# Kernel optimization log

Measured on AMD Instinct MI355X. Metric: run time of the kernel, lower is better.

Reference implementation:

```python
import jax, jax.numpy as jnp
import numpy as np


def setup_inputs() -> dict:
    key = jax.random.key(0)
    k1, k2 = jax.random.split(key)
    N, B, E, H = 2048, 8, 256, 512
    x = jax.random.normal(k1, (N, B, E), dtype=jnp.float32)
    h = jax.random.normal(k2, (N, B, H), dtype=jnp.float32)
    return {"x": x, "h": h}


def reference(x, h):
    # x: (N, B, E), h: (N, B, H)
    H = h.shape[-1]
    xt = jnp.transpose(x, (1, 0, 2))            # (B, N, E)
    norm = jnp.linalg.norm(xt, axis=2, keepdims=True)  # (B, N, 1)
    xn = xt / norm
    # cosine-similarity scores, softmax over keys (last dim)
    scores = jax.nn.softmax(jnp.einsum('bie,bje->bij', xn, xn), axis=2)  # (B, N, N)
    ht = jnp.transpose(h, (1, 0, 2))            # (B, N, H)
    # The original expands scores/h over an H-fold dim, bmm's, and sums;
    # that equals H * (scores @ h). Keep the H factor for faithfulness
    # (it cancels in the global-norm division below).
    g = H * jnp.einsum('bij,bjh->bih', scores, ht)  # (B, N, H)
    g = jnp.transpose(g, (1, 0, 2))             # (N, B, H)
    return g / jnp.linalg.norm(g)
```

## Files before the change

kernel.cpp:

```cpp
#include <hip/hip_runtime.h>

#define N_TOK 2048
#define B_SZ  8
#define E_DIM 256
#define H_DIM 512
#define ITERS (N_TOK / 32)
#define QROWS 64

typedef __attribute__((ext_vector_type(8))) short bf16x8;
typedef __attribute__((ext_vector_type(4))) float f32x4;
typedef __attribute__((ext_vector_type(4))) unsigned short u16x4;

__device__ __forceinline__ unsigned short f2bf(float f) {
    union { float f; unsigned u; } v; v.f = f;
    unsigned r = v.u + 0x7FFF + ((v.u >> 16) & 1);
    return (unsigned short)(r >> 16);
}
__device__ __forceinline__ float bf2f(unsigned short b) {
    union { unsigned u; float f; } v; v.u = ((unsigned)b) << 16;
    return v.f;
}

__global__ void prep_kernel(const float* __restrict__ x,
                            const float* __restrict__ hptr,
                            unsigned short* __restrict__ Xn,
                            unsigned short* __restrict__ Vp,
                            float* __restrict__ sumsq) {
    int bid = blockIdx.x;
    int t = threadIdx.x;
    if (bid == 0 && t == 0) *sumsq = 0.0f;
    if (bid < (N_TOK * B_SZ) / 4) {
        int w = t >> 6, lane = t & 63;
        int r = bid * 4 + w;
        int n = r >> 3, b = r & 7;
        float4 v = *(const float4*)(x + (size_t)r * E_DIM + lane * 4);
        float s = v.x * v.x + v.y * v.y + v.z * v.z + v.w * v.w;
        #pragma unroll
        for (int o = 32; o > 0; o >>= 1) s += __shfl_xor(s, o);
        float rn = 1.0f / sqrtf(s);
        u16x4 pk;
        pk[0] = f2bf(v.x * rn); pk[1] = f2bf(v.y * rn);
        pk[2] = f2bf(v.z * rn); pk[3] = f2bf(v.w * rn);
        int u = lane >> 1, half = lane & 1;
        *(u16x4*)(Xn + ((size_t)b * N_TOK + n) * E_DIM
                     + (size_t)((u ^ (n & 7)) * 8 + half * 4)) = pk;
    } else {
        int lin = bid - (N_TOK * B_SZ) / 4;
        int jb = lin & 63, hb = (lin >> 6) & 15, b = lin >> 10;
        __shared__ __attribute__((aligned(16))) float tile[32][36];
        int j0 = jb * 32, h0 = hb * 32;
        {
            int j = t >> 3, c = (t & 7) * 4;
            float4 v = *(const float4*)(hptr +
                ((size_t)(j0 + j) * B_SZ + b) * H_DIM + h0 + c);
            *(float4*)(&tile[j][c]) = v;
        }
        __syncthreads();
        size_t base = ((size_t)b * (N_TOK / 32) + jb) * (H_DIM * 32);
        int hcl = t >> 3, jg = (t >> 1) & 3, half = t & 1;
        int hc = h0 + hcl;
        u16x4 pk;
        #pragma unroll
        for (int k = 0; k < 4; k++)
            pk[k] = f2bf(tile[jg * 8 + half * 4 + k][hcl]);
        *(u16x4*)(Vp + base + (size_t)(hc * 4 + (jg ^ ((hcl >> 1) & 3))) * 8
                     + half * 4) = pk;
    }
}

#define PT_STRIDE 40

__launch_bounds__(256, 2)
__global__ void flash_kernel(const unsigned short* __restrict__ Xn,
                             const unsigned short* __restrict__ Vp,
                             float* __restrict__ out,
                             float* __restrict__ sumsq) {
    __shared__ __attribute__((aligned(16))) unsigned short Kbuf[2][32 * 256];
    __shared__ __attribute__((aligned(16))) unsigned short Pt[4][16 * PT_STRIDE];
    __shared__ float Lred[4][16];

    int b  = blockIdx.x;
    int q0 = blockIdx.y * QROWS;
    int z  = blockIdx.z;
    int t = threadIdx.x;
    int w = t >> 6, lane = t & 63;
    int quad = lane >> 4, nm = lane & 15;

    const unsigned short* Kbase = Xn + (size_t)b * N_TOK * E_DIM;
    const unsigned short* Qrow =
        Xn + ((size_t)b * N_TOK + q0 + w * 16 + nm) * E_DIM;
    const unsigned short* Vtile0 = Vp + (size_t)b * (N_TOK / 32) * (H_DIM * 32);
    int col0 = z * 256 + w * 64;

    bf16x8 qf[8];
    #pragma unroll
    for (int ec = 0; ec < 8; ec++)
        qf[ec] = *(const bf16x8*)(Qrow + (size_t)(((ec * 4 + quad) ^ (nm & 7)) * 8));

    f32x4 O[4][4];
    #pragma unroll
    for (int i = 0; i < 4; i++)
        #pragma unroll
        for (int j = 0; j < 4; j++) O[i][j] = (f32x4){0.f, 0.f, 0.f, 0.f};
    float l_lane[4];
    #pragma unroll
    for (int r = 0; r < 4; r++) l_lane[r] = 0.0f;

    auto stage = [&](int tile, int buf) {
        const unsigned short* src0 = Kbase + (size_t)tile * 32 * E_DIM;
        #pragma unroll
        for (int k = 0; k < 4; k++) {
            int chunk = w * 4 + k;
            __builtin_amdgcn_global_load_lds(
                (const __attribute__((address_space(1))) unsigned int*)
                    (src0 + (size_t)chunk * 512 + lane * 8),
                (__attribute__((address_space(3))) unsigned int*)
                    (&Kbuf[buf][chunk * 512]),
                16, 0, 0);
        }
    };

    stage(0, 0);
    int vswz = (quad ^ ((nm >> 1) & 3)) * 8;

    for (int it = 0; it < ITERS; ++it) {
        __syncthreads();
        int cur = it & 1;

        const unsigned short* Vt = Vtile0 + (size_t)it * (H_DIM * 32);
        bf16x8 vf[4];
        #pragma unroll
        for (int tt = 0; tt < 4; tt++) {
            int hc = col0 + tt * 16 + nm;
            vf[tt] = *(const bf16x8*)(Vt + (size_t)(hc * 4) * 8 + vswz);
        }

        if (it + 1 < ITERS) stage(it + 1, cur ^ 1);
        const unsigned short* KB = &Kbuf[cur][0];

        f32x4 sa = (f32x4){0.f,0.f,0.f,0.f}, sb = (f32x4){0.f,0.f,0.f,0.f};
        #pragma unroll
        for (int ec = 0; ec < 8; ec++) {
            int u = ((ec * 4 + quad) ^ (nm & 7)) * 8;
            bf16x8 kf0 = *(const bf16x8*)(KB + nm * 256 + u);
            bf16x8 kf1 = *(const bf16x8*)(KB + (16 + nm) * 256 + u);
            sa = __builtin_amdgcn_mfma_f32_16x16x32_bf16(qf[ec], kf0, sa, 0, 0, 0);
            sb = __builtin_amdgcn_mfma_f32_16x16x32_bf16(qf[ec], kf1, sb, 0, 0, 0);
        }

        #pragma unroll
        for (int r = 0; r < 4; r++) {
            unsigned short pb0 = f2bf(__expf(sa[r] - 1.0f));
            unsigned short pb1 = f2bf(__expf(sb[r] - 1.0f));
            l_lane[r] += bf2f(pb0) + bf2f(pb1);
            Pt[w][(quad * 4 + r) * PT_STRIDE + nm]      = pb0;
            Pt[w][(quad * 4 + r) * PT_STRIDE + 16 + nm] = pb1;
        }

        asm volatile("s_waitcnt lgkmcnt(0)" ::: "memory");
        __builtin_amdgcn_s_barrier();
        asm volatile("" ::: "memory");

        #pragma unroll
        for (int rg = 0; rg < 4; rg++) {
            bf16x8 pf = *(const bf16x8*)(&Pt[rg][nm * PT_STRIDE + quad * 8]);
            #pragma unroll
            for (int ct = 0; ct < 4; ct++)
                O[rg][ct] = __builtin_amdgcn_mfma_f32_16x16x32_bf16(
                    pf, vf[ct], O[rg][ct], 0, 0, 0);
        }
    }

    float lv[4];
    #pragma unroll
    for (int r = 0; r < 4; r++) {
        float v = l_lane[r];
        #pragma unroll
        for (int o = 1; o < 16; o <<= 1) v += __shfl_xor(v, o);
        lv[r] = v;
    }
    if (nm == 0) {
        #pragma unroll
        for (int r = 0; r < 4; r++) Lred[w][quad * 4 + r] = lv[r];
    }
    __syncthreads();

    float ss = 0.0f;
    #pragma unroll
    for (int rg = 0; rg < 4; rg++) {
        float linv[4];
        #pragma unroll
        for (int r = 0; r < 4; r++)
            linv[r] = 1.0f / Lred[rg][quad * 4 + r];
        #pragma unroll
        for (int ct = 0; ct < 4; ct++) {
            #pragma unroll
            for (int r = 0; r < 4; r++) {
                float val = O[rg][ct][r] * linv[r];
                int row = q0 + rg * 16 + quad * 4 + r;
                int col = col0 + ct * 16 + nm;
                out[((size_t)row * B_SZ + b) * H_DIM + col] = val;
                ss += val * val;
            }
        }
    }
    #pragma unroll
    for (int o = 1; o < 64; o <<= 1) ss += __shfl_xor(ss, o);
    if (lane == 0) atomicAdd(sumsq, ss);
}

__global__ void scale_kernel(float* __restrict__ out,
                             const float* __restrict__ sumsq) {
    size_t idx = ((size_t)blockIdx.x * blockDim.x + threadIdx.x) * 4;
    float rs = 1.0f / sqrtf(*sumsq);
    float4 v = *(float4*)(out + idx);
    v.x *= rs; v.y *= rs; v.z *= rs; v.w *= rs;
    *(float4*)(out + idx) = v;
}

extern "C" void kernel_launch(void* const* d_in, const int* in_sizes, int n_in,
                              void* d_out, int out_size, void* d_ws, size_t ws_size,
                              hipStream_t stream) {
    const float* x = (const float*)d_in[0];
    const float* h = (const float*)d_in[1];
    float* out = (float*)d_out;

    unsigned short* Xn = (unsigned short*)d_ws;
    unsigned short* Vp = Xn + (size_t)B_SZ * N_TOK * E_DIM;
    float* sumsq = (float*)(Vp + (size_t)B_SZ * N_TOK * H_DIM);

    prep_kernel<<<(N_TOK * B_SZ) / 4 + (N_TOK / 32) * (H_DIM / 32) * B_SZ,
                  256, 0, stream>>>(x, h, Xn, Vp, sumsq);
    flash_kernel<<<dim3(B_SZ, N_TOK / QROWS, 2), 256, 0, stream>>>(
        Xn, Vp, out, sumsq);
    scale_kernel<<<out_size / (4 * 256), 256, 0, stream>>>(out, sumsq);
}
```

Before: 206.2 us.

## Triple-buffer K tiles and prefetch V fragments one iteration ahead

The K tile buffer in LDS grows from double to triple buffering, so tiles are staged two iterations ahead. The per-iteration __syncthreads is replaced by an explicit vmcnt wait plus s_barrier. V fragments for the next iteration are loaded into alternating register sets, using a macro unrolled twice. The goal is to hide global-load latency behind the MFMA work. The cost is extra LDS (48KB for K), which may hurt occupancy at two blocks per CU, higher register pressure, and a fragile hand-counted vmcnt that must stay correct.

```diff
diff --git a/kernel.cpp b/kernel.cpp
--- a/kernel.cpp
+++ b/kernel.cpp
@@ -75,7 +75,7 @@
                              const unsigned short* __restrict__ Vp,
                              float* __restrict__ out,
                              float* __restrict__ sumsq) {
-    __shared__ __attribute__((aligned(16))) unsigned short Kbuf[2][32 * 256];
+    __shared__ __attribute__((aligned(16))) unsigned short Kbuf[3][32 * 256];
     __shared__ __attribute__((aligned(16))) unsigned short Pt[4][16 * PT_STRIDE];
     __shared__ float Lred[4][16];
 
@@ -120,56 +120,76 @@
         }
     };
 
+    int vswz = (quad ^ ((nm >> 1) & 3)) * 8;
+
+    bf16x8 vfA[4], vfB[4];
     stage(0, 0);
-    int vswz = (quad ^ ((nm >> 1) & 3)) * 8;
-
-    for (int it = 0; it < ITERS; ++it) {
-        __syncthreads();
-        int cur = it & 1;
-
-        const unsigned short* Vt = Vtile0 + (size_t)it * (H_DIM * 32);
-        bf16x8 vf[4];
+    {
+        const unsigned short* Vt = Vtile0;
         #pragma unroll
         for (int tt = 0; tt < 4; tt++) {
             int hc = col0 + tt * 16 + nm;
-            vf[tt] = *(const bf16x8*)(Vt + (size_t)(hc * 4) * 8 + vswz);
-        }
-
-        if (it + 1 < ITERS) stage(it + 1, cur ^ 1);
-        const unsigned short* KB = &Kbuf[cur][0];
-
-        f32x4 sa = (f32x4){0.f,0.f,0.f,0.f}, sb = (f32x4){0.f,0.f,0.f,0.f};
-        #pragma unroll
-        for (int ec = 0; ec < 8; ec++) {
-            int u = ((ec * 4 + quad) ^ (nm & 7)) * 8;
-            bf16x8 kf0 = *(const bf16x8*)(KB + nm * 256 + u);
-            bf16x8 kf1 = *(const bf16x8*)(KB + (16 + nm) * 256 + u);
-            sa = __builtin_amdgcn_mfma_f32_16x16x32_bf16(qf[ec], kf0, sa, 0, 0, 0);
-            sb = __builtin_amdgcn_mfma_f32_16x16x32_bf16(qf[ec], kf1, sb, 0, 0, 0);
-        }
-
-        #pragma unroll
-        for (int r = 0; r < 4; r++) {
-            unsigned short pb0 = f2bf(__expf(sa[r] - 1.0f));
-            unsigned short pb1 = f2bf(__expf(sb[r] - 1.0f));
-            l_lane[r] += bf2f(pb0) + bf2f(pb1);
-            Pt[w][(quad * 4 + r) * PT_STRIDE + nm]      = pb0;
-            Pt[w][(quad * 4 + r) * PT_STRIDE + 16 + nm] = pb1;
-        }
-
-        asm volatile("s_waitcnt lgkmcnt(0)" ::: "memory");
-        __builtin_amdgcn_s_barrier();
-        asm volatile("" ::: "memory");
-
-        #pragma unroll
-        for (int rg = 0; rg < 4; rg++) {
-            bf16x8 pf = *(const bf16x8*)(&Pt[rg][nm * PT_STRIDE + quad * 8]);
-            #pragma unroll
-            for (int ct = 0; ct < 4; ct++)
-                O[rg][ct] = __builtin_amdgcn_mfma_f32_16x16x32_bf16(
-                    pf, vf[ct], O[rg][ct], 0, 0, 0);
-        }
-    }
+            vfA[tt] = *(const bf16x8*)(Vt + (size_t)(hc * 4) * 8 + vswz);
+        }
+    }
+    stage(1, 1);
+
+#define FLASH_BODY(IT, VC, VN) do {                                            \
+           \
+    if ((IT) < ITERS - 1) asm volatile("s_waitcnt vmcnt(8)" ::: "memory");     \
+    else                  asm volatile("s_waitcnt vmcnt(4)" ::: "memory");     \
+    __builtin_amdgcn_s_barrier();                                              \
+    asm volatile("" ::: "memory");                                             \
+    const unsigned short* KB = &Kbuf[(IT) % 3][0];                             \
+           \
+    f32x4 sa = (f32x4){0.f,0.f,0.f,0.f}, sb = (f32x4){0.f,0.f,0.f,0.f};        \
+    _Pragma("unroll")                                                          \
+    for (int ec = 0; ec < 8; ec++) {                                           \
+        int u = ((ec * 4 + quad) ^ (nm & 7)) * 8;                              \
+        bf16x8 kf0 = *(const bf16x8*)(KB + nm * 256 + u);                      \
+        bf16x8 kf1 = *(const bf16x8*)(KB + (16 + nm) * 256 + u);               \
+        sa = __builtin_amdgcn_mfma_f32_16x16x32_bf16(qf[ec], kf0, sa, 0,0,0);  \
+        sb = __builtin_amdgcn_mfma_f32_16x16x32_bf16(qf[ec], kf1, sb, 0,0,0);  \
+    }                                                                          \
+               \
+    _Pragma("unroll")                                                          \
+    for (int r = 0; r < 4; r++) {                                              \
+        unsigned short pb0 = f2bf(__expf(sa[r] - 1.0f));                       \
+        unsigned short pb1 = f2bf(__expf(sb[r] - 1.0f));                       \
+        l_lane[r] += bf2f(pb0) + bf2f(pb1);                                    \
+        Pt[w][(quad * 4 + r) * PT_STRIDE + nm]      = pb0;                     \
+        Pt[w][(quad * 4 + r) * PT_STRIDE + 16 + nm] = pb1;                     \
+    }                                                                          \
+    asm volatile("s_waitcnt lgkmcnt(0)" ::: "memory");                         \
+    __builtin_amdgcn_s_barrier();                                              \
+    asm volatile("" ::: "memory");                                             \
+       \
+             \
+    _Pragma("unroll")                                                          \
+    for (int rg = 0; rg < 4; rg++) {                                           \
+        bf16x8 pf = *(const bf16x8*)(&Pt[rg][nm * PT_STRIDE + quad * 8]);      \
+        _Pragma("unroll")                                                      \
+        for (int ct = 0; ct < 4; ct++)                                         \
+            O[rg][ct] = __builtin_amdgcn_mfma_f32_16x16x32_bf16(               \
+                pf, VC[ct], O[rg][ct], 0, 0, 0);                               \
+    }                                                                          \
+              \
+    if ((IT) + 1 < ITERS) {                                                    \
+        const unsigned short* Vt = Vtile0 + (size_t)((IT)+1) * (H_DIM * 32);   \
+        _Pragma("unroll")                                                      \
+        for (int tt = 0; tt < 4; tt++) {                                       \
+            int hc = col0 + tt * 16 + nm;                                      \
+            VN[tt] = *(const bf16x8*)(Vt + (size_t)(hc * 4) * 8 + vswz);       \
+        }                                                                      \
+    }                                                                          \
+    if ((IT) + 2 < ITERS) stage((IT) + 2, ((IT) + 2) % 3);                     \
+} while (0)
+
+    for (int itp = 0; itp < ITERS; itp += 2) {
+        FLASH_BODY(itp,     vfA, vfB);
+        FLASH_BODY(itp + 1, vfB, vfA);
+    }
+#undef FLASH_BODY
 
     float lv[4];
     #pragma unroll
```

After: 217.0 us. 1.05x slower.

## Fuse prep, flash attention and scaling into one persistent kernel with grid barriers

Applied to the files above, without the earlier changes.

Merges the three kernels into one 512-block persistent kernel that uses atomic grid-wide barriers between the prep, attention and global-normalisation phases, with a memset to zero the accumulator and barrier counters. This is meant to remove two kernel launch gaps and the tail effects between dependent phases. In exchange it relies on all 512 blocks being co-resident (two per CU), and the spin barrier has a timeout break that could silently break correctness if blocks are not all resident. The prep work is also redistributed, with each block handling more rows serially.

```diff
diff --git a/kernel.cpp b/kernel.cpp
--- a/kernel.cpp
+++ b/kernel.cpp
@@ -6,6 +6,8 @@
 #define H_DIM 512
 #define ITERS (N_TOK / 32)
 #define QROWS 64
+#define PT_STRIDE 40
+#define NBLK 512
 
 typedef __attribute__((ext_vector_type(8))) short bf16x8;
 typedef __attribute__((ext_vector_type(4))) float f32x4;
@@ -21,201 +23,231 @@
     return v.f;
 }
 
-__global__ void prep_kernel(const float* __restrict__ x,
+__device__ __forceinline__ void grid_bar(int* bar) {
+    __syncthreads();
+    if (threadIdx.x == 0) {
+        __threadfence();
+        __hip_atomic_fetch_add(bar, 1, __ATOMIC_ACQ_REL, __HIP_MEMORY_SCOPE_AGENT);
+        int spins = 0;
+        while (__hip_atomic_load(bar, __ATOMIC_ACQUIRE,
+                                 __HIP_MEMORY_SCOPE_AGENT) < NBLK) {
+            __builtin_amdgcn_s_sleep(8);
+            if (++spins > (1 << 16)) break;
+        }
+        __threadfence();
+    }
+    __syncthreads();
+}
+
+__launch_bounds__(256, 2)
+__global__ void mega_kernel(const float* __restrict__ x,
                             const float* __restrict__ hptr,
                             unsigned short* __restrict__ Xn,
                             unsigned short* __restrict__ Vp,
-                            float* __restrict__ sumsq) {
-    int bid = blockIdx.x;
-    int t = threadIdx.x;
-    if (bid == 0 && t == 0) *sumsq = 0.0f;
-    if (bid < (N_TOK * B_SZ) / 4) {
-        int w = t >> 6, lane = t & 63;
-        int r = bid * 4 + w;
-        int n = r >> 3, b = r & 7;
-        float4 v = *(const float4*)(x + (size_t)r * E_DIM + lane * 4);
-        float s = v.x * v.x + v.y * v.y + v.z * v.z + v.w * v.w;
-        #pragma unroll
-        for (int o = 32; o > 0; o >>= 1) s += __shfl_xor(s, o);
-        float rn = 1.0f / sqrtf(s);
-        u16x4 pk;
-        pk[0] = f2bf(v.x * rn); pk[1] = f2bf(v.y * rn);
-        pk[2] = f2bf(v.z * rn); pk[3] = f2bf(v.w * rn);
-        int u = lane >> 1, half = lane & 1;
-        *(u16x4*)(Xn + ((size_t)b * N_TOK + n) * E_DIM
-                     + (size_t)((u ^ (n & 7)) * 8 + half * 4)) = pk;
-    } else {
-        int lin = bid - (N_TOK * B_SZ) / 4;
-        int jb = lin & 63, hb = (lin >> 6) & 15, b = lin >> 10;
-        __shared__ __attribute__((aligned(16))) float tile[32][36];
-        int j0 = jb * 32, h0 = hb * 32;
-        {
-            int j = t >> 3, c = (t & 7) * 4;
-            float4 v = *(const float4*)(hptr +
-                ((size_t)(j0 + j) * B_SZ + b) * H_DIM + h0 + c);
-            *(float4*)(&tile[j][c]) = v;
-        }
-        __syncthreads();
-        size_t base = ((size_t)b * (N_TOK / 32) + jb) * (H_DIM * 32);
-        int hcl = t >> 3, jg = (t >> 1) & 3, half = t & 1;
-        int hc = h0 + hcl;
-        u16x4 pk;
-        #pragma unroll
-        for (int k = 0; k < 4; k++)
-            pk[k] = f2bf(tile[jg * 8 + half * 4 + k][hcl]);
-        *(u16x4*)(Vp + base + (size_t)(hc * 4 + (jg ^ ((hcl >> 1) & 3))) * 8
-                     + half * 4) = pk;
-    }
-}
-
-#define PT_STRIDE 40
-
-__launch_bounds__(256, 2)
-__global__ void flash_kernel(const unsigned short* __restrict__ Xn,
-                             const unsigned short* __restrict__ Vp,
-                             float* __restrict__ out,
-                             float* __restrict__ sumsq) {
+                            float* __restrict__ out,
+                            float* __restrict__ sumsq,
+                            int* __restrict__ bars) {
     __shared__ __attribute__((aligned(16))) unsigned short Kbuf[2][32 * 256];
     __shared__ __attribute__((aligned(16))) unsigned short Pt[4][16 * PT_STRIDE];
     __shared__ float Lred[4][16];
-
-    int b  = blockIdx.x;
-    int q0 = blockIdx.y * QROWS;
-    int z  = blockIdx.z;
+    __shared__ __attribute__((aligned(16))) float tile[32][36];
+
+    int bid = blockIdx.x;
     int t = threadIdx.x;
+    int b = bid & 7;
+    int y = bid >> 3;
     int w = t >> 6, lane = t & 63;
     int quad = lane >> 4, nm = lane & 15;
 
-    const unsigned short* Kbase = Xn + (size_t)b * N_TOK * E_DIM;
-    const unsigned short* Qrow =
-        Xn + ((size_t)b * N_TOK + q0 + w * 16 + nm) * E_DIM;
-    const unsigned short* Vtile0 = Vp + (size_t)b * (N_TOK / 32) * (H_DIM * 32);
-    int col0 = z * 256 + w * 64;
-
-    bf16x8 qf[8];
-    #pragma unroll
-    for (int ec = 0; ec < 8; ec++)
-        qf[ec] = *(const bf16x8*)(Qrow + (size_t)(((ec * 4 + quad) ^ (nm & 7)) * 8));
-
-    f32x4 O[4][4];
-    #pragma unroll
-    for (int i = 0; i < 4; i++)
-        #pragma unroll
-        for (int j = 0; j < 4; j++) O[i][j] = (f32x4){0.f, 0.f, 0.f, 0.f};
-    float l_lane[4];
-    #pragma unroll
-    for (int r = 0; r < 4; r++) l_lane[r] = 0.0f;
-
-    auto stage = [&](int tile, int buf) {
-        const unsigned short* src0 = Kbase + (size_t)tile * 32 * E_DIM;
-        #pragma unroll
-        for (int k = 0; k < 4; k++) {
-            int chunk = w * 4 + k;
-            __builtin_amdgcn_global_load_lds(
-                (const __attribute__((address_space(1))) unsigned int*)
-                    (src0 + (size_t)chunk * 512 + lane * 8),
-                (__attribute__((address_space(3))) unsigned int*)
-                    (&Kbuf[buf][chunk * 512]),
-                16, 0, 0);
-        }
-    };
-
-    stage(0, 0);
-    int vswz = (quad ^ ((nm >> 1) & 3)) * 8;
-
-    for (int it = 0; it < ITERS; ++it) {
+    {
+        int idx = y * 4 + w;
+        #pragma unroll
+        for (int k = 0; k < 8; k++) {
+            int n = idx + 256 * k;
+            int r = n * 8 + b;
+            float4 v = *(const float4*)(x + (size_t)r * E_DIM + lane * 4);
+            float s = v.x * v.x + v.y * v.y + v.z * v.z + v.w * v.w;
+            #pragma unroll
+            for (int o = 32; o > 0; o >>= 1) s += __shfl_xor(s, o);
+            float rn = 1.0f / sqrtf(s);
+            u16x4 pk;
+            pk[0] = f2bf(v.x * rn); pk[1] = f2bf(v.y * rn);
+            pk[2] = f2bf(v.z * rn); pk[3] = f2bf(v.w * rn);
+            int u = lane >> 1, half = lane & 1;
+            *(u16x4*)(Xn + ((size_t)b * N_TOK + n) * E_DIM
+                         + (size_t)((u ^ (n & 7)) * 8 + half * 4)) = pk;
+        }
+    }
+
+    {
+        int jb = y, j0 = jb * 32;
+        for (int hb = 0; hb < 16; hb++) {
+            int h0 = hb * 32;
+            {
+                int j = t >> 3, c = (t & 7) * 4;
+                float4 v = *(const float4*)(hptr +
+                    ((size_t)(j0 + j) * B_SZ + b) * H_DIM + h0 + c);
+                *(float4*)(&tile[j][c]) = v;
+            }
+            __syncthreads();
+            size_t base = ((size_t)b * (N_TOK / 32) + jb) * (H_DIM * 32);
+            int hcl = t >> 3, jg = (t >> 1) & 3, half = t & 1;
+            int hc = h0 + hcl;
+            u16x4 pk;
+            #pragma unroll
+            for (int k = 0; k < 4; k++)
+                pk[k] = f2bf(tile[jg * 8 + half * 4 + k][hcl]);
+            *(u16x4*)(Vp + base + (size_t)(hc * 4 + (jg ^ ((hcl >> 1) & 3))) * 8
+                         + half * 4) = pk;
+            __syncthreads();
+        }
+    }
+
+    grid_bar(&bars[0]);
+
+    {
+        int qy = y & 31;
+        int z  = bid >> 8;
+        int q0 = qy * QROWS;
+
+        const unsigned short* Kbase = Xn + (size_t)b * N_TOK * E_DIM;
+        const unsigned short* Qrow =
+            Xn + ((size_t)b * N_TOK + q0 + w * 16 + nm) * E_DIM;
+        const unsigned short* Vtile0 =
+            Vp + (size_t)b * (N_TOK / 32) * (H_DIM * 32);
+        int col0 = z * 256 + w * 64;
+
+        bf16x8 qf[8];
+        #pragma unroll
+        for (int ec = 0; ec < 8; ec++)
+            qf[ec] = *(const bf16x8*)(Qrow +
+                (size_t)(((ec * 4 + quad) ^ (nm & 7)) * 8));
+
+        f32x4 O[4][4];
+        #pragma unroll
+        for (int i = 0; i < 4; i++)
+            #pragma unroll
+            for (int j = 0; j < 4; j++) O[i][j] = (f32x4){0.f, 0.f, 0.f, 0.f};
+        float l_lane[4];
+        #pragma unroll
+        for (int r = 0; r < 4; r++) l_lane[r] = 0.0f;
+
+        auto stage = [&](int tile_, int buf) {
+            const unsigned short* src0 = Kbase + (size_t)tile_ * 32 * E_DIM;
+            #pragma unroll
+            for (int k = 0; k < 4; k++) {
+                int chunk = w * 4 + k;
+                __builtin_amdgcn_global_load_lds(
+                    (const __attribute__((address_space(1))) unsigned int*)
+                        (src0 + (size_t)chunk * 512 + lane * 8),
+                    (__attribute__((address_space(3))) unsigned int*)
+                        (&Kbuf[buf][chunk * 512]),
+                    16, 0, 0);
+            }
+        };
+
+        stage(0, 0);
+        int vswz = (quad ^ ((nm >> 1) & 3)) * 8;
+
+        for (int it = 0; it < ITERS; ++it) {
+            __syncthreads();
+            int cur = it & 1;
+
+            const unsigned short* Vt = Vtile0 + (size_t)it * (H_DIM * 32);
+            bf16x8 vf[4];
+            #pragma unroll
+            for (int tt = 0; tt < 4; tt++) {
+                int hc = col0 + tt * 16 + nm;
+                vf[tt] = *(const bf16x8*)(Vt + (size_t)(hc * 4) * 8 + vswz);
+            }
+
+            if (it + 1 < ITERS) stage(it + 1, cur ^ 1);
+            const unsigned short* KB = &Kbuf[cur][0];
+
+            f32x4 sa = (f32x4){0.f,0.f,0.f,0.f}, sb = (f32x4){0.f,0.f,0.f,0.f};
+            #pragma unroll
+            for (int ec = 0; ec < 8; ec++) {
+                int u = ((ec * 4 + quad) ^ (nm & 7)) * 8;
+                bf16x8 kf0 = *(const bf16x8*)(KB + nm * 256 + u);
+                bf16x8 kf1 = *(const bf16x8*)(KB + (16 + nm) * 256 + u);
+                sa = __builtin_amdgcn_mfma_f32_16x16x32_bf16(qf[ec], kf0, sa, 0, 0, 0);
+                sb = __builtin_amdgcn_mfma_f32_16x16x32_bf16(qf[ec], kf1, sb, 0, 0, 0);
+            }
+
+            #pragma unroll
+            for (int r = 0; r < 4; r++) {
+                unsigned short pb0 = f2bf(__expf(sa[r] - 1.0f));
+                unsigned short pb1 = f2bf(__expf(sb[r] - 1.0f));
+                l_lane[r] += bf2f(pb0) + bf2f(pb1);
+                Pt[w][(quad * 4 + r) * PT_STRIDE + nm]      = pb0;
+                Pt[w][(quad * 4 + r) * PT_STRIDE + 16 + nm] = pb1;
+            }
+
+            asm volatile("s_waitcnt lgkmcnt(0)" ::: "memory");
+            __builtin_amdgcn_s_barrier();
+            asm volatile("" ::: "memory");
+
+            #pragma unroll
+            for (int rg = 0; rg < 4; rg++) {
+                bf16x8 pf = *(const bf16x8*)(&Pt[rg][nm * PT_STRIDE + quad * 8]);
+                #pragma unroll
+                for (int ct = 0; ct < 4; ct++)
+                    O[rg][ct] = __builtin_amdgcn_mfma_f32_16x16x32_bf16(
+                        pf, vf[ct], O[rg][ct], 0, 0, 0);
+            }
+        }
+
+        float lv[4];
+        #pragma unroll
+        for (int r = 0; r < 4; r++) {
+            float v = l_lane[r];
+            #pragma unroll
+            for (int o = 1; o < 16; o <<= 1) v += __shfl_xor(v, o);
+            lv[r] = v;
+        }
+        if (nm == 0) {
+            #pragma unroll
+            for (int r = 0; r < 4; r++) Lred[w][quad * 4 + r] = lv[r];
+        }
         __syncthreads();
-        int cur = it & 1;
-
-        const unsigned short* Vt = Vtile0 + (size_t)it * (H_DIM * 32);
-        bf16x8 vf[4];
-        #pragma unroll
-        for (int tt = 0; tt < 4; tt++) {
-            int hc = col0 + tt * 16 + nm;
-            vf[tt] = *(const bf16x8*)(Vt + (size_t)(hc * 4) * 8 + vswz);
-        }
-
-        if (it + 1 < ITERS) stage(it + 1, cur ^ 1);
-        const unsigned short* KB = &Kbuf[cur][0];
-
-        f32x4 sa = (f32x4){0.f,0.f,0.f,0.f}, sb = (f32x4){0.f,0.f,0.f,0.f};
-        #pragma unroll
-        for (int ec = 0; ec < 8; ec++) {
-            int u = ((ec * 4 + quad) ^ (nm & 7)) * 8;
-            bf16x8 kf0 = *(const bf16x8*)(KB + nm * 256 + u);
-            bf16x8 kf1 = *(const bf16x8*)(KB + (16 + nm) * 256 + u);
-            sa = __builtin_amdgcn_mfma_f32_16x16x32_bf16(qf[ec], kf0, sa, 0, 0, 0);
-            sb = __builtin_amdgcn_mfma_f32_16x16x32_bf16(qf[ec], kf1, sb, 0, 0, 0);
-        }
-
-        #pragma unroll
-        for (int r = 0; r < 4; r++) {
-            unsigned short pb0 = f2bf(__expf(sa[r] - 1.0f));
-            unsigned short pb1 = f2bf(__expf(sb[r] - 1.0f));
-            l_lane[r] += bf2f(pb0) + bf2f(pb1);
-            Pt[w][(quad * 4 + r) * PT_STRIDE + nm]      = pb0;
-            Pt[w][(quad * 4 + r) * PT_STRIDE + 16 + nm] = pb1;
-        }
-
-        asm volatile("s_waitcnt lgkmcnt(0)" ::: "memory");
-        __builtin_amdgcn_s_barrier();
-        asm volatile("" ::: "memory");
-
+
+        float ss = 0.0f;
         #pragma unroll
         for (int rg = 0; rg < 4; rg++) {
-            bf16x8 pf = *(const bf16x8*)(&Pt[rg][nm * PT_STRIDE + quad * 8]);
-            #pragma unroll
-            for (int ct = 0; ct < 4; ct++)
-                O[rg][ct] = __builtin_amdgcn_mfma_f32_16x16x32_bf16(
-                    pf, vf[ct], O[rg][ct], 0, 0, 0);
-        }
-    }
-
-    float lv[4];
-    #pragma unroll
-    for (int r = 0; r < 4; r++) {
-        float v = l_lane[r];
-        #pragma unroll
-        for (int o = 1; o < 16; o <<= 1) v += __shfl_xor(v, o);
-        lv[r] = v;
-    }
-    if (nm == 0) {
-        #pragma unroll
-        for (int r = 0; r < 4; r++) Lred[w][quad * 4 + r] = lv[r];
-    }
-    __syncthreads();
-
-    float ss = 0.0f;
-    #pragma unroll
-    for (int rg = 0; rg < 4; rg++) {
-        float linv[4];
-        #pragma unroll
-        for (int r = 0; r < 4; r++)
-            linv[r] = 1.0f / Lred[rg][quad * 4 + r];
-        #pragma unroll
-        for (int ct = 0; ct < 4; ct++) {
-            #pragma unroll
-            for (int r = 0; r < 4; r++) {
-                float val = O[rg][ct][r] * linv[r];
-                int row = q0 + rg * 16 + quad * 4 + r;
-                int col = col0 + ct * 16 + nm;
-                out[((size_t)row * B_SZ + b) * H_DIM + col] = val;
-                ss += val * val;
-            }
-        }
-    }
-    #pragma unroll
-    for (int o = 1; o < 64; o <<= 1) ss += __shfl_xor(ss, o);
-    if (lane == 0) atomicAdd(sumsq, ss);
-}
-
-__global__ void scale_kernel(float* __restrict__ out,
-                             const float* __restrict__ sumsq) {
-    size_t idx = ((size_t)blockIdx.x * blockDim.x + threadIdx.x) * 4;
-    float rs = 1.0f / sqrtf(*sumsq);
-    float4 v = *(float4*)(out + idx);
-    v.x *= rs; v.y *= rs; v.z *= rs; v.w *= rs;
-    *(float4*)(out + idx) = v;
+            float linv[4];
+            #pragma unroll
+            for (int r = 0; r < 4; r++)
+                linv[r] = 1.0f / Lred[rg][quad * 4 + r];
+            #pragma unroll
+            for (int ct = 0; ct < 4; ct++) {
+                #pragma unroll
+                for (int r = 0; r < 4; r++) {
+                    float val = O[rg][ct][r] * linv[r];
+                    int row = q0 + rg * 16 + quad * 4 + r;
+                    int col = col0 + ct * 16 + nm;
+                    out[((size_t)row * B_SZ + b) * H_DIM + col] = val;
+                    ss += val * val;
+                }
+            }
+        }
+        #pragma unroll
+        for (int o = 1; o < 64; o <<= 1) ss += __shfl_xor(ss, o);
+        if (lane == 0) atomicAdd(sumsq, ss);
+    }
+
+    grid_bar(&bars[1]);
+
+    {
+        float rs = 1.0f / sqrtf(*sumsq);
+        #pragma unroll
+        for (int i = 0; i < 16; i++) {
+            size_t i4 = (size_t)i * (NBLK * 256) + (size_t)bid * 256 + t;
+            size_t g = i4 * 4;
+            float4 v = *(float4*)(out + g);
+            v.x *= rs; v.y *= rs; v.z *= rs; v.w *= rs;
+            *(float4*)(out + g) = v;
+        }
+    }
 }
 
 extern "C" void kernel_launch(void* const* d_in, const int* in_sizes, int n_in,
@@ -228,10 +260,8 @@
     unsigned short* Xn = (unsigned short*)d_ws;
     unsigned short* Vp = Xn + (size_t)B_SZ * N_TOK * E_DIM;
     float* sumsq = (float*)(Vp + (size_t)B_SZ * N_TOK * H_DIM);
-
-    prep_kernel<<<(N_TOK * B_SZ) / 4 + (N_TOK / 32) * (H_DIM / 32) * B_SZ,
-                  256, 0, stream>>>(x, h, Xn, Vp, sumsq);
-    flash_kernel<<<dim3(B_SZ, N_TOK / QROWS, 2), 256, 0, stream>>>(
-        Xn, Vp, out, sumsq);
-    scale_kernel<<<out_size / (4 * 256), 256, 0, stream>>>(out, sumsq);
-}
+    int* bars = (int*)(sumsq + 1);
+
+    hipMemsetAsync(sumsq, 0, 12, stream);
+    mega_kernel<<<NBLK, 256, 0, stream>>>(x, h, Xn, Vp, out, sumsq, bars);
+}
```

Measured after the change: 449.1 us. 2.18x slower.
